# Performance work log

Measured on AMD Instinct MI355X. Metric: run time of the kernel, lower is better.

## Reference

```python
import jax, jax.numpy as jnp
import numpy as np

N, E = 50000, 400000
IN_CH, HID, HEADS, EDGE_DIM = 128, 64, 4, 3
NEG_SLOPE = 0.2


def gatv2_conv(x, src, dst, edge_attr, Wl, Wr, We, att, bias):
    # x: [N, F_in]; Wl/Wr: [H*C, F_in]; We: [H*C, edge_dim]; att: [H, C]; bias: [C]
    H, C = att.shape
    n = x.shape[0]
    xl = (x @ Wl.T).reshape(n, H, C)   # source-side transform (lin_l)
    xr = (x @ Wr.T).reshape(n, H, C)   # target-side transform (lin_r)
    e = (edge_attr @ We.T).reshape(-1, H, C)
    z = jax.nn.leaky_relu(xl[src] + xr[dst] + e, NEG_SLOPE)  # [E,H,C]
    alpha = jnp.einsum('ehc,hc->eh', z, att)                 # [E,H]
    # segment softmax over incoming edges per destination node
    amax = jax.ops.segment_max(alpha, dst, num_segments=n)
    alpha = jnp.exp(alpha - amax[dst])
    denom = jax.ops.segment_sum(alpha, dst, num_segments=n)
    alpha = alpha / (denom[dst] + 1e-16)
    msg = xl[src] * alpha[:, :, None]                        # [E,H,C]
    out = jax.ops.segment_sum(msg, dst, num_segments=n)      # [N,H,C]
    return out.mean(axis=1) + bias                           # concat=False -> head mean


def setup_inputs() -> dict:
    key = jax.random.key(0)
    ks = jax.random.split(key, 16)
    s = 0.1
    return {
        'x': jax.random.normal(ks[0], (N, IN_CH), jnp.float32),
        'edge_index': jax.random.randint(ks[1], (2, E), 0, N, jnp.int32),
        'edge_attr': jax.random.normal(ks[2], (E, EDGE_DIM), jnp.float32),
        'Wl1': jax.random.normal(ks[3], (HEADS * HID, IN_CH), jnp.float32) * s,
        'Wr1': jax.random.normal(ks[4], (HEADS * HID, IN_CH), jnp.float32) * s,
        'We1': jax.random.normal(ks[5], (HEADS * HID, EDGE_DIM), jnp.float32) * s,
        'att1': jax.random.normal(ks[6], (HEADS, HID), jnp.float32) * s,
        'b1': jnp.zeros((HID,), jnp.float32),
        'Wl2': jax.random.normal(ks[7], (HEADS * HID, HID), jnp.float32) * s,
        'Wr2': jax.random.normal(ks[8], (HEADS * HID, HID), jnp.float32) * s,
        'We2': jax.random.normal(ks[9], (HEADS * HID, EDGE_DIM), jnp.float32) * s,
        'att2': jax.random.normal(ks[10], (HEADS, HID), jnp.float32) * s,
        'b2': jnp.zeros((HID,), jnp.float32),
        'prelu_w': jnp.full((HID,), 0.25, jnp.float32),
    }


def reference(x, edge_index, edge_attr, Wl1, Wr1, We1, att1, b1, Wl2, Wr2, We2, att2, b2, prelu_w):
    src, dst = edge_index[0], edge_index[1]
    h = gatv2_conv(x, src, dst, edge_attr, Wl1, Wr1, We1, att1, b1)
    h = gatv2_conv(h, src, dst, edge_attr, Wl2, Wr2, We2, att2, b2)
    return jnp.where(h >= 0, h, prelu_w * h)  # PReLU, per-channel weight
```

## Files before the change

### kernel.cpp

```cpp
#include <hip/hip_runtime.h>
#include <hip/hip_bf16.h>

#define HC 256

typedef __attribute__((ext_vector_type(8))) short bf16x8;
typedef __attribute__((ext_vector_type(4))) float f32x4;
typedef __attribute__((ext_vector_type(2))) float f32x2;

__device__ __forceinline__ void gl_lds16(const void* g, void* l) {
  __builtin_amdgcn_global_load_lds(
      (const __attribute__((address_space(1))) unsigned int*)g,
      (__attribute__((address_space(3))) unsigned int*)l, 16, 0, 0);
}

__device__ __forceinline__ void split_w_one(const float* Wl, const float* Wr,
                                            ushort* WT, int F, int idx) {
  int col = idx / F, f = idx - col * F;
  float v = (col < 256) ? Wl[col * F + f] : Wr[(col - 256) * F + f];
  __hip_bfloat16 h = __float2bfloat16(v);
  __hip_bfloat16 l = __float2bfloat16(v - __bfloat162float(h));
  ushort* row = WT + (size_t)col * 3 * F;
  row[f] = *(ushort*)&h;
  row[F + f] = *(ushort*)&l;
  row[2 * F + f] = *(ushort*)&h;
}

__global__ void k_weights_deg(const float* __restrict__ Wl1, const float* __restrict__ Wr1,
                              ushort* __restrict__ WT1, const float* __restrict__ Wl2,
                              const float* __restrict__ Wr2, ushort* __restrict__ WT2,
                              int* __restrict__ deg, int n) {
  int idx = blockIdx.x * blockDim.x + threadIdx.x;
  const int t1 = 512 * 128, t2 = 512 * 64;
  if (idx < t1) {
    split_w_one(Wl1, Wr1, WT1, 128, idx);
  } else if (idx < t1 + t2) {
    split_w_one(Wl2, Wr2, WT2, 64, idx - t1);
  } else if (idx < t1 + t2 + n) {
    deg[idx - t1 - t2] = 0;
  }
}

template <int F>
__global__ __launch_bounds__(256) void gemm_mfma(const ushort* __restrict__ A2,
                                                 const ushort* __restrict__ WT,
                                                 ushort* __restrict__ xlb,
                                                 ushort* __restrict__ xrb, int n_nodes) {
  constexpr int KC = 3 * F;
  __shared__ __align__(16) ushort As[128 * 64];
  __shared__ __align__(16) ushort Bs[128 * 64];
  const int tid = threadIdx.x;
  const int wv = tid >> 6, lane = tid & 63;
  const int m16 = lane & 15, quad = lane >> 4;
  const int col0 = blockIdx.x * 128;
  const int row0 = blockIdx.y * 128;
  const int wm = (wv >> 1) * 64, wn = (wv & 1) * 64;
  const bool is_xl = (col0 < 256);
  const int nstep = is_xl ? (3 * F) / 64 : F / 64;

  f32x4 acc[4][4];
#pragma unroll
  for (int i = 0; i < 4; ++i)
#pragma unroll
    for (int j = 0; j < 4; ++j) acc[i][j] = (f32x4){0.f, 0.f, 0.f, 0.f};

  for (int s = 0; s < nstep; ++s) {
    const int khat = s * 64;
    const int asrc = (khat < F) ? khat : khat - F;
    __syncthreads();
#pragma unroll
    for (int t = 0; t < 4; ++t) {
      const int sl16 = tid + 256 * t;
      const int row = sl16 >> 3, sl = sl16 & 7;
      const int gch = sl ^ (row & 7);
      const int grow = row0 + row;
      if (grow < n_nodes)
        gl_lds16(A2 + (size_t)grow * (2 * F) + asrc + gch * 8, As + sl16 * 8);
      gl_lds16(WT + (size_t)(col0 + row) * KC + khat + gch * 8, Bs + sl16 * 8);
    }
    __syncthreads();
#pragma unroll
    for (int kh = 0; kh < 2; ++kh) {
      bf16x8 af[4], bf[4];
#pragma unroll
      for (int i = 0; i < 4; ++i) {
        const int row = wm + i * 16 + m16;
        const int slot = (kh * 4 + quad) ^ (row & 7);
        af[i] = *(bf16x8*)&As[row * 64 + slot * 8];
      }
#pragma unroll
      for (int j = 0; j < 4; ++j) {
        const int col = wn + j * 16 + m16;
        const int slot = (kh * 4 + quad) ^ (col & 7);
        bf[j] = *(bf16x8*)&Bs[col * 64 + slot * 8];
      }
#pragma unroll
      for (int i = 0; i < 4; ++i)
#pragma unroll
        for (int j = 0; j < 4; ++j)
          acc[i][j] =
              __builtin_amdgcn_mfma_f32_16x16x32_bf16(af[i], bf[j], acc[i][j], 0, 0, 0);
    }
  }
#pragma unroll
  for (int i = 0; i < 4; ++i) {
#pragma unroll
    for (int r = 0; r < 4; ++r) {
      const int grow = row0 + wm + i * 16 + quad * 4 + r;
      if (grow < n_nodes) {
#pragma unroll
        for (int j = 0; j < 4; ++j) {
          const float v = acc[i][j][r];
          const int col = col0 + wn + j * 16 + m16;
          __hip_bfloat16 h = __float2bfloat16(v);
          if (is_xl)
            xlb[(size_t)grow * 256 + col] = *(ushort*)&h;
          else
            xrb[(size_t)grow * 256 + (col - 256)] = *(ushort*)&h;
        }
      }
    }
  }
}

__global__ void k_hist(const int* __restrict__ ei, int* __restrict__ deg, int E_) {
  int e = blockIdx.x * blockDim.x + threadIdx.x;
  if (e < E_) atomicAdd(&deg[ei[E_ + e]], 1);
}

__global__ void k_scan_local(const int* __restrict__ deg, int* __restrict__ rowstart,
                             int* __restrict__ partial, int n) {
  __shared__ int a[256], b[256];
  const int t = threadIdx.x;
  const int i = blockIdx.x * 256 + t;
  const int v = (i < n) ? deg[i] : 0;
  a[t] = v;
  __syncthreads();
  int* cur = a;
  int* nxt = b;
  for (int off = 1; off < 256; off <<= 1) {
    int x = cur[t];
    if (t >= off) x += cur[t - off];
    nxt[t] = x;
    __syncthreads();
    int* tmp = cur; cur = nxt; nxt = tmp;
  }
  const int incl = cur[t];
  if (i < n) rowstart[i] = incl - v;
  if (t == 255) partial[blockIdx.x] = incl;
}

__global__ void k_scan_partial(int* __restrict__ partial, int nblk,
                               int* __restrict__ ssrc, float4* __restrict__ sea, int E_) {
  __shared__ int a[256], b[256];
  const int t = threadIdx.x;
  if (t < 8) {
    ssrc[E_ + t] = 0;
    sea[E_ + t] = make_float4(0.f, 0.f, 0.f, 0.f);
  }
  const int v = (t < nblk) ? partial[t] : 0;
  a[t] = v;
  __syncthreads();
  int* cur = a;
  int* nxt = b;
  for (int off = 1; off < 256; off <<= 1) {
    int x = cur[t];
    if (t >= off) x += cur[t - off];
    nxt[t] = x;
    __syncthreads();
    int* tmp = cur; cur = nxt; nxt = tmp;
  }
  if (t < nblk) partial[t] = cur[t] - v;
}

__global__ void k_add_off(int* __restrict__ rowstart, int* __restrict__ cursor,
                          const int* __restrict__ partial, int n, int E_) {
  int i = blockIdx.x * blockDim.x + threadIdx.x;
  if (i < n) {
    int v = rowstart[i] + partial[i >> 8];
    rowstart[i] = v;
    cursor[i] = v;
  }
  if (i == 0) rowstart[n] = E_;
}

__global__ void k_prep(const float* __restrict__ x, ushort* __restrict__ A2,
                       const int* __restrict__ ei, const float* __restrict__ ea,
                       int* __restrict__ cursor, int* __restrict__ ssrc,
                       float4* __restrict__ sea, int n, int E_) {
  const int nx4 = n * 128 / 4;
  int idx = blockIdx.x * blockDim.x + threadIdx.x;
  if (idx < nx4) {
    int row = idx >> 5, q = idx & 31;
    float4 v = ((const float4*)x)[idx];
    float vv[4] = {v.x, v.y, v.z, v.w};
    ushort hb[4], lb[4];
#pragma unroll
    for (int j = 0; j < 4; ++j) {
      __hip_bfloat16 h = __float2bfloat16(vv[j]);
      hb[j] = *(ushort*)&h;
      __hip_bfloat16 l = __float2bfloat16(vv[j] - __bfloat162float(h));
      lb[j] = *(ushort*)&l;
    }
    ushort* rp = A2 + (size_t)row * 256;
    *(ushort4*)(rp + q * 4) = make_ushort4(hb[0], hb[1], hb[2], hb[3]);
    *(ushort4*)(rp + 128 + q * 4) = make_ushort4(lb[0], lb[1], lb[2], lb[3]);
  } else {
    int e = idx - nx4;
    if (e < E_) {
      int dst = ei[E_ + e];
      int pos = atomicAdd(&cursor[dst], 1);
      ssrc[pos] = ei[e];
      sea[pos] = make_float4(ea[e * 3], ea[e * 3 + 1], ea[e * 3 + 2], 0.f);
    }
  }
}

__device__ __forceinline__ f32x2 vmax2(f32x2 a, f32x2 b) {
  return (f32x2){fmaxf(a.x, b.x), fmaxf(a.y, b.y)};
}
__device__ __forceinline__ f32x2 vmin2(f32x2 a, f32x2 b) {
  return (f32x2){fminf(a.x, b.x), fminf(a.y, b.y)};
}

__device__ __forceinline__ void edge_step(
    const ushort4& lu, const float4& eav, const f32x2* we0, const f32x2* we1,
    const f32x2* we2, const f32x2* at, const f32x2* xrl, f32x2& num01,
    f32x2& num23, float& den) {
  f32x2 lav0, lav1;
  lav0.x = __uint_as_float((unsigned)lu.x << 16);
  lav0.y = __uint_as_float((unsigned)lu.y << 16);
  lav1.x = __uint_as_float((unsigned)lu.z << 16);
  lav1.y = __uint_as_float((unsigned)lu.w << 16);
  const f32x2 zero = {0.f, 0.f};
  const f32x2 slope = {0.2f, 0.2f};
  f32x2 pv = zero;
#pragma unroll
  for (int j = 0; j < 2; ++j) {
    f32x2 la = (j == 0) ? lav0 : lav1;
    f32x2 ev = we0[j] * eav.x + we1[j] * eav.y + we2[j] * eav.z;
    f32x2 s = la + xrl[j] + ev;
    f32x2 z = vmax2(s, zero) + slope * vmin2(s, zero);
    pv = pv + z * at[j];
  }
  float p = pv.x + pv.y;
  p += __shfl_xor(p, 1);
  p += __shfl_xor(p, 2);
  p += __shfl_xor(p, 4);
  p += __shfl_xor(p, 8);
  const float w = __expf(p);
  den += w;
  num01 = num01 + (f32x2){w, w} * lav0;
  num23 = num23 + (f32x2){w, w} * lav1;
}

template <int MODE>
__global__ __launch_bounds__(256) void fused_attn(
    const ushort* __restrict__ xlb, const ushort* __restrict__ xrb,
    const int* __restrict__ rowstart, const int* __restrict__ ssrc,
    const float4* __restrict__ sea, const float* __restrict__ We,
    const float* __restrict__ att, const float* __restrict__ bias,
    const float* __restrict__ pw, float* __restrict__ out,
    ushort* __restrict__ outs, int n) {
  const int lane = threadIdx.x & 63;
  const int d =
      __builtin_amdgcn_readfirstlane((blockIdx.x * blockDim.x + threadIdx.x) >> 6);
  if (d >= n) return;
  f32x2 we0[2], we1[2], we2[2], at[2];
#pragma unroll
  for (int j = 0; j < 4; ++j) {
    int r = 4 * lane + j;
    ((float*)we0)[j] = We[r * 3 + 0];
    ((float*)we1)[j] = We[r * 3 + 1];
    ((float*)we2)[j] = We[r * 3 + 2];
    ((float*)at)[j] = att[r];
  }
  const ushort4* xlb4 = (const ushort4*)xlb;
  const ushort4 xu = ((const ushort4*)xrb)[(unsigned)(d * 64) + lane];
  f32x2 xrl[2];
  xrl[0].x = __uint_as_float((unsigned)xu.x << 16);
  xrl[0].y = __uint_as_float((unsigned)xu.y << 16);
  xrl[1].x = __uint_as_float((unsigned)xu.z << 16);
  xrl[1].y = __uint_as_float((unsigned)xu.w << 16);

  int pos = rowstart[d];
  const int end = rowstart[d + 1];
  f32x2 num01 = {0.f, 0.f}, num23 = {0.f, 0.f};
  float den = 0.f;

  if (pos < end) {
    int s0 = ssrc[pos], s1 = ssrc[pos + 1];
    ushort4 g0 = xlb4[(unsigned)(s0 * 64) + lane];
    ushort4 g1 = xlb4[(unsigned)(s1 * 64) + lane];
    float4 e0 = sea[pos], e1 = sea[pos + 1];
    int sn0 = ssrc[pos + 2], sn1 = ssrc[pos + 3];

    while (pos + 2 <= end) {
      ushort4 h0 = xlb4[(unsigned)(sn0 * 64) + lane];
      ushort4 h1 = xlb4[(unsigned)(sn1 * 64) + lane];
      float4 f0 = sea[pos + 2], f1 = sea[pos + 3];
      sn0 = ssrc[pos + 4];
      sn1 = ssrc[pos + 5];
      edge_step(g0, e0, we0, we1, we2, at, xrl, num01, num23, den);
      edge_step(g1, e1, we0, we1, we2, at, xrl, num01, num23, den);
      g0 = h0; g1 = h1; e0 = f0; e1 = f1;
      pos += 2;
    }
    if (pos < end)
      edge_step(g0, e0, we0, we1, we2, at, xrl, num01, num23, den);
  }

  const float inv = 1.f / (den + 1e-16f);
  float4 r;
  r.x = num01.x * inv;
  r.y = num01.y * inv;
  r.z = num23.x * inv;
  r.w = num23.y * inv;
  r.x += __shfl_xor(r.x, 16);
  r.y += __shfl_xor(r.y, 16);
  r.z += __shfl_xor(r.z, 16);
  r.w += __shfl_xor(r.w, 16);
  r.x += __shfl_xor(r.x, 32);
  r.y += __shfl_xor(r.y, 32);
  r.z += __shfl_xor(r.z, 32);
  r.w += __shfl_xor(r.w, 32);
  if (lane < 16) {
    const int c = 4 * lane;
    float o[4];
    o[0] = 0.25f * r.x + bias[c + 0];
    o[1] = 0.25f * r.y + bias[c + 1];
    o[2] = 0.25f * r.z + bias[c + 2];
    o[3] = 0.25f * r.w + bias[c + 3];
    if (MODE == 1) {
#pragma unroll
      for (int j = 0; j < 4; ++j) o[j] = (o[j] >= 0.f) ? o[j] : pw[c + j] * o[j];
      ((float4*)out)[(size_t)d * 16 + lane] = make_float4(o[0], o[1], o[2], o[3]);
    } else {
      ushort hb[4], lb[4];
#pragma unroll
      for (int j = 0; j < 4; ++j) {
        __hip_bfloat16 h = __float2bfloat16(o[j]);
        hb[j] = *(ushort*)&h;
        __hip_bfloat16 l = __float2bfloat16(o[j] - __bfloat162float(h));
        lb[j] = *(ushort*)&l;
      }
      *(ushort4*)(outs + (size_t)d * 128 + c) = make_ushort4(hb[0], hb[1], hb[2], hb[3]);
      *(ushort4*)(outs + (size_t)d * 128 + 64 + c) =
          make_ushort4(lb[0], lb[1], lb[2], lb[3]);
    }
  }
}

extern "C" void kernel_launch(void* const* d_in, const int* in_sizes, int n_in,
                              void* d_out, int out_size, void* d_ws, size_t ws_size,
                              hipStream_t stream) {
  const float* x    = (const float*)d_in[0];
  const int*   ei   = (const int*)d_in[1];
  const float* ea   = (const float*)d_in[2];
  const float* Wl1  = (const float*)d_in[3];
  const float* Wr1  = (const float*)d_in[4];
  const float* We1  = (const float*)d_in[5];
  const float* att1 = (const float*)d_in[6];
  const float* b1   = (const float*)d_in[7];
  const float* Wl2  = (const float*)d_in[8];
  const float* Wr2  = (const float*)d_in[9];
  const float* We2  = (const float*)d_in[10];
  const float* att2 = (const float*)d_in[11];
  const float* b2   = (const float*)d_in[12];
  const float* pw   = (const float*)d_in[13];
  const int N_ = in_sizes[0] / 128;
  const int E_ = in_sizes[1] / 2;
  float* out = (float*)d_out;

  char* w = (char*)d_ws;
  auto alloc = [&](size_t bytes) {
    char* p = w;
    w += (bytes + 255) & ~size_t(255);
    return p;
  };
  ushort* xlb      = (ushort*)alloc((size_t)N_ * 256 * 2);
  ushort* xrb      = (ushort*)alloc((size_t)N_ * 256 * 2);
  ushort* A2x      = (ushort*)alloc((size_t)N_ * 256 * 2);
  ushort* h2       = (ushort*)alloc((size_t)N_ * 128 * 2);
  int*    ssrc     = (int*)alloc((size_t)(E_ + 8) * 4);
  float4* sea      = (float4*)alloc((size_t)(E_ + 8) * 16);
  int*    deg      = (int*)alloc((size_t)N_ * 4);
  int*    rowstart = (int*)alloc((size_t)(N_ + 1) * 4);
  int*    cursor   = (int*)alloc((size_t)N_ * 4);
  int*    partial  = (int*)alloc(256 * 4);
  ushort* WT1      = (ushort*)alloc((size_t)512 * 384 * 2);
  ushort* WT2      = (ushort*)alloc((size_t)512 * 192 * 2);

  const int wtot = 512 * 128 + 512 * 64 + N_;
  k_weights_deg<<<(wtot + 255) / 256, 256, 0, stream>>>(Wl1, Wr1, WT1, Wl2, Wr2, WT2,
                                                        deg, N_);

  const int nblk = (N_ + 255) / 256;
  k_hist<<<(E_ + 255) / 256, 256, 0, stream>>>(ei, deg, E_);
  k_scan_local<<<nblk, 256, 0, stream>>>(deg, rowstart, partial, N_);
  k_scan_partial<<<1, 256, 0, stream>>>(partial, nblk, ssrc, sea, E_);
  k_add_off<<<nblk, 256, 0, stream>>>(rowstart, cursor, partial, N_, E_);
  const int ptot = N_ * 128 / 4 + E_;
  k_prep<<<(ptot + 255) / 256, 256, 0, stream>>>(x, A2x, ei, ea, cursor, ssrc, sea,
                                                 N_, E_);

  const dim3 GG(4, (N_ + 127) / 128);
  const int FB = (N_ + 3) / 4;

  gemm_mfma<128><<<GG, 256, 0, stream>>>(A2x, WT1, xlb, xrb, N_);
  fused_attn<0><<<FB, 256, 0, stream>>>(xlb, xrb, rowstart, ssrc, sea, We1, att1,
                                        b1, pw, nullptr, h2, N_);
  gemm_mfma<64><<<GG, 256, 0, stream>>>(h2, WT2, xlb, xrb, N_);
  fused_attn<1><<<FB, 256, 0, stream>>>(xlb, xrb, rowstart, ssrc, sea, We2, att2,
                                        b2, pw, out, nullptr, N_);
}
```

Before: 301.8 us.

## Drop split-bf16 GEMM compensation and process multiple nodes per wavefront in attention

Removes the hi/lo bf16 splitting of activations and weights, so both GEMMs run a plain single-bf16 product with a third of the K steps (layer 1) and half the A-operand traffic, and intermediate h2 is stored as single bf16. The attention kernel now launches a fixed grid of 8192 wavefronts, each looping over a chunk of destination nodes, and hoists the bias and PReLU weight loads out of the loop. The cost removed is extra MFMA work, conversion work and memory traffic, in exchange for lower numerical accuracy, which may exceed tolerance. The fixed grid also gives less latency hiding per node.

```diff
diff --git a/kernel.cpp b/kernel.cpp
--- a/kernel.cpp
+++ b/kernel.cpp
@@ -13,16 +13,12 @@
       (__attribute__((address_space(3))) unsigned int*)l, 16, 0, 0);
 }
 
-__device__ __forceinline__ void split_w_one(const float* Wl, const float* Wr,
-                                            ushort* WT, int F, int idx) {
+__device__ __forceinline__ void cast_w_one(const float* Wl, const float* Wr,
+                                           ushort* WT, int F, int idx) {
   int col = idx / F, f = idx - col * F;
   float v = (col < 256) ? Wl[col * F + f] : Wr[(col - 256) * F + f];
   __hip_bfloat16 h = __float2bfloat16(v);
-  __hip_bfloat16 l = __float2bfloat16(v - __bfloat162float(h));
-  ushort* row = WT + (size_t)col * 3 * F;
-  row[f] = *(ushort*)&h;
-  row[F + f] = *(ushort*)&l;
-  row[2 * F + f] = *(ushort*)&h;
+  WT[(size_t)col * F + f] = *(ushort*)&h;
 }
 
 __global__ void k_weights_deg(const float* __restrict__ Wl1, const float* __restrict__ Wr1,
@@ -32,20 +28,20 @@
   int idx = blockIdx.x * blockDim.x + threadIdx.x;
   const int t1 = 512 * 128, t2 = 512 * 64;
   if (idx < t1) {
-    split_w_one(Wl1, Wr1, WT1, 128, idx);
+    cast_w_one(Wl1, Wr1, WT1, 128, idx);
   } else if (idx < t1 + t2) {
-    split_w_one(Wl2, Wr2, WT2, 64, idx - t1);
+    cast_w_one(Wl2, Wr2, WT2, 64, idx - t1);
   } else if (idx < t1 + t2 + n) {
     deg[idx - t1 - t2] = 0;
   }
 }
 
 template <int F>
-__global__ __launch_bounds__(256) void gemm_mfma(const ushort* __restrict__ A2,
+__global__ __launch_bounds__(256) void gemm_mfma(const ushort* __restrict__ A,
                                                  const ushort* __restrict__ WT,
                                                  ushort* __restrict__ xlb,
                                                  ushort* __restrict__ xrb, int n_nodes) {
-  constexpr int KC = 3 * F;
+  constexpr int NSTEP = F / 64;
   __shared__ __align__(16) ushort As[128 * 64];
   __shared__ __align__(16) ushort Bs[128 * 64];
   const int tid = threadIdx.x;
@@ -54,8 +50,6 @@
   const int col0 = blockIdx.x * 128;
   const int row0 = blockIdx.y * 128;
   const int wm = (wv >> 1) * 64, wn = (wv & 1) * 64;
-  const bool is_xl = (col0 < 256);
-  const int nstep = is_xl ? (3 * F) / 64 : F / 64;
 
   f32x4 acc[4][4];
 #pragma unroll
@@ -63,9 +57,9 @@
 #pragma unroll
     for (int j = 0; j < 4; ++j) acc[i][j] = (f32x4){0.f, 0.f, 0.f, 0.f};
 
-  for (int s = 0; s < nstep; ++s) {
+#pragma unroll
+  for (int s = 0; s < NSTEP; ++s) {
     const int khat = s * 64;
-    const int asrc = (khat < F) ? khat : khat - F;
     __syncthreads();
 #pragma unroll
     for (int t = 0; t < 4; ++t) {
@@ -74,8 +68,8 @@
       const int gch = sl ^ (row & 7);
       const int grow = row0 + row;
       if (grow < n_nodes)
-        gl_lds16(A2 + (size_t)grow * (2 * F) + asrc + gch * 8, As + sl16 * 8);
-      gl_lds16(WT + (size_t)(col0 + row) * KC + khat + gch * 8, Bs + sl16 * 8);
+        gl_lds16(A + (size_t)grow * F + khat + gch * 8, As + sl16 * 8);
+      gl_lds16(WT + (size_t)(col0 + row) * F + khat + gch * 8, Bs + sl16 * 8);
     }
     __syncthreads();
 #pragma unroll
@@ -101,6 +95,7 @@
               __builtin_amdgcn_mfma_f32_16x16x32_bf16(af[i], bf[j], acc[i][j], 0, 0, 0);
     }
   }
+  const bool is_xl = (col0 < 256);
 #pragma unroll
   for (int i = 0; i < 4; ++i) {
 #pragma unroll
@@ -183,29 +178,25 @@
   if (i == 0) rowstart[n] = E_;
 }
 
-__global__ void k_prep(const float* __restrict__ x, ushort* __restrict__ A2,
+__global__ void k_prep(const float* __restrict__ x, ushort* __restrict__ A,
                        const int* __restrict__ ei, const float* __restrict__ ea,
                        int* __restrict__ cursor, int* __restrict__ ssrc,
                        float4* __restrict__ sea, int n, int E_) {
-  const int nx4 = n * 128 / 4;
+  const int nx8 = n * 16;
   int idx = blockIdx.x * blockDim.x + threadIdx.x;
-  if (idx < nx4) {
-    int row = idx >> 5, q = idx & 31;
-    float4 v = ((const float4*)x)[idx];
-    float vv[4] = {v.x, v.y, v.z, v.w};
-    ushort hb[4], lb[4];
-#pragma unroll
-    for (int j = 0; j < 4; ++j) {
+  if (idx < nx8) {
+    const float4* xp = (const float4*)x + (size_t)idx * 2;
+    float4 v0 = xp[0], v1 = xp[1];
+    float vv[8] = {v0.x, v0.y, v0.z, v0.w, v1.x, v1.y, v1.z, v1.w};
+    __align__(16) ushort hb[8];
+#pragma unroll
+    for (int j = 0; j < 8; ++j) {
       __hip_bfloat16 h = __float2bfloat16(vv[j]);
       hb[j] = *(ushort*)&h;
-      __hip_bfloat16 l = __float2bfloat16(vv[j] - __bfloat162float(h));
-      lb[j] = *(ushort*)&l;
-    }
-    ushort* rp = A2 + (size_t)row * 256;
-    *(ushort4*)(rp + q * 4) = make_ushort4(hb[0], hb[1], hb[2], hb[3]);
-    *(ushort4*)(rp + 128 + q * 4) = make_ushort4(lb[0], lb[1], lb[2], lb[3]);
+    }
+    *(int4*)(A + (size_t)idx * 8) = *(int4*)hb;
   } else {
-    int e = idx - nx4;
+    int e = idx - nx8;
     if (e < E_) {
       int dst = ei[E_ + e];
       int pos = atomicAdd(&cursor[dst], 1);
@@ -260,11 +251,14 @@
     const float4* __restrict__ sea, const float* __restrict__ We,
     const float* __restrict__ att, const float* __restrict__ bias,
     const float* __restrict__ pw, float* __restrict__ out,
-    ushort* __restrict__ outs, int n) {
+    ushort* __restrict__ outs, int n, int chunk) {
   const int lane = threadIdx.x & 63;
-  const int d =
+  const int wid =
       __builtin_amdgcn_readfirstlane((blockIdx.x * blockDim.x + threadIdx.x) >> 6);
-  if (d >= n) return;
+  const int d0 = wid * chunk;
+  if (d0 >= n) return;
+  const int d1 = min(d0 + chunk, n);
+
   f32x2 we0[2], we1[2], we2[2], at[2];
 #pragma unroll
   for (int j = 0; j < 4; ++j) {
@@ -274,78 +268,81 @@
     ((float*)we2)[j] = We[r * 3 + 2];
     ((float*)at)[j] = att[r];
   }
+  const float4 bias4 = ((const float4*)bias)[lane & 15];
+  float4 pw4 = {0.f, 0.f, 0.f, 0.f};
+  if (MODE == 1) pw4 = ((const float4*)pw)[lane & 15];
   const ushort4* xlb4 = (const ushort4*)xlb;
-  const ushort4 xu = ((const ushort4*)xrb)[(unsigned)(d * 64) + lane];
-  f32x2 xrl[2];
-  xrl[0].x = __uint_as_float((unsigned)xu.x << 16);
-  xrl[0].y = __uint_as_float((unsigned)xu.y << 16);
-  xrl[1].x = __uint_as_float((unsigned)xu.z << 16);
-  xrl[1].y = __uint_as_float((unsigned)xu.w << 16);
-
-  int pos = rowstart[d];
-  const int end = rowstart[d + 1];
-  f32x2 num01 = {0.f, 0.f}, num23 = {0.f, 0.f};
-  float den = 0.f;
-
-  if (pos < end) {
-    int s0 = ssrc[pos], s1 = ssrc[pos + 1];
-    ushort4 g0 = xlb4[(unsigned)(s0 * 64) + lane];
-    ushort4 g1 = xlb4[(unsigned)(s1 * 64) + lane];
-    float4 e0 = sea[pos], e1 = sea[pos + 1];
-    int sn0 = ssrc[pos + 2], sn1 = ssrc[pos + 3];
-
-    while (pos + 2 <= end) {
-      ushort4 h0 = xlb4[(unsigned)(sn0 * 64) + lane];
-      ushort4 h1 = xlb4[(unsigned)(sn1 * 64) + lane];
-      float4 f0 = sea[pos + 2], f1 = sea[pos + 3];
-      sn0 = ssrc[pos + 4];
-      sn1 = ssrc[pos + 5];
-      edge_step(g0, e0, we0, we1, we2, at, xrl, num01, num23, den);
-      edge_step(g1, e1, we0, we1, we2, at, xrl, num01, num23, den);
-      g0 = h0; g1 = h1; e0 = f0; e1 = f1;
-      pos += 2;
-    }
-    if (pos < end)
-      edge_step(g0, e0, we0, we1, we2, at, xrl, num01, num23, den);
-  }
-
-  const float inv = 1.f / (den + 1e-16f);
-  float4 r;
-  r.x = num01.x * inv;
-  r.y = num01.y * inv;
-  r.z = num23.x * inv;
-  r.w = num23.y * inv;
-  r.x += __shfl_xor(r.x, 16);
-  r.y += __shfl_xor(r.y, 16);
-  r.z += __shfl_xor(r.z, 16);
-  r.w += __shfl_xor(r.w, 16);
-  r.x += __shfl_xor(r.x, 32);
-  r.y += __shfl_xor(r.y, 32);
-  r.z += __shfl_xor(r.z, 32);
-  r.w += __shfl_xor(r.w, 32);
-  if (lane < 16) {
-    const int c = 4 * lane;
-    float o[4];
-    o[0] = 0.25f * r.x + bias[c + 0];
-    o[1] = 0.25f * r.y + bias[c + 1];
-    o[2] = 0.25f * r.z + bias[c + 2];
-    o[3] = 0.25f * r.w + bias[c + 3];
-    if (MODE == 1) {
-#pragma unroll
-      for (int j = 0; j < 4; ++j) o[j] = (o[j] >= 0.f) ? o[j] : pw[c + j] * o[j];
-      ((float4*)out)[(size_t)d * 16 + lane] = make_float4(o[0], o[1], o[2], o[3]);
-    } else {
-      ushort hb[4], lb[4];
-#pragma unroll
-      for (int j = 0; j < 4; ++j) {
-        __hip_bfloat16 h = __float2bfloat16(o[j]);
-        hb[j] = *(ushort*)&h;
-        __hip_bfloat16 l = __float2bfloat16(o[j] - __bfloat162float(h));
-        lb[j] = *(ushort*)&l;
+
+  for (int d = d0; d < d1; ++d) {
+    const ushort4 xu = ((const ushort4*)xrb)[(unsigned)(d * 64) + lane];
+    f32x2 xrl[2];
+    xrl[0].x = __uint_as_float((unsigned)xu.x << 16);
+    xrl[0].y = __uint_as_float((unsigned)xu.y << 16);
+    xrl[1].x = __uint_as_float((unsigned)xu.z << 16);
+    xrl[1].y = __uint_as_float((unsigned)xu.w << 16);
+
+    int pos = rowstart[d];
+    const int end = rowstart[d + 1];
+    f32x2 num01 = {0.f, 0.f}, num23 = {0.f, 0.f};
+    float den = 0.f;
+
+    if (pos < end) {
+      int s0 = ssrc[pos], s1 = ssrc[pos + 1];
+      ushort4 g0 = xlb4[(unsigned)(s0 * 64) + lane];
+      ushort4 g1 = xlb4[(unsigned)(s1 * 64) + lane];
+      float4 e0 = sea[pos], e1 = sea[pos + 1];
+      int sn0 = ssrc[pos + 2], sn1 = ssrc[pos + 3];
+
+      while (pos + 2 <= end) {
+        ushort4 h0 = xlb4[(unsigned)(sn0 * 64) + lane];
+        ushort4 h1 = xlb4[(unsigned)(sn1 * 64) + lane];
+        float4 f0 = sea[pos + 2], f1 = sea[pos + 3];
+        sn0 = ssrc[pos + 4];
+        sn1 = ssrc[pos + 5];
+        edge_step(g0, e0, we0, we1, we2, at, xrl, num01, num23, den);
+        edge_step(g1, e1, we0, we1, we2, at, xrl, num01, num23, den);
+        g0 = h0; g1 = h1; e0 = f0; e1 = f1;
+        pos += 2;
       }
-      *(ushort4*)(outs + (size_t)d * 128 + c) = make_ushort4(hb[0], hb[1], hb[2], hb[3]);
-      *(ushort4*)(outs + (size_t)d * 128 + 64 + c) =
-          make_ushort4(lb[0], lb[1], lb[2], lb[3]);
+      if (pos < end)
+        edge_step(g0, e0, we0, we1, we2, at, xrl, num01, num23, den);
+    }
+
+    const float inv = 1.f / (den + 1e-16f);
+    float4 r;
+    r.x = num01.x * inv;
+    r.y = num01.y * inv;
+    r.z = num23.x * inv;
+    r.w = num23.y * inv;
+    r.x += __shfl_xor(r.x, 16);
+    r.y += __shfl_xor(r.y, 16);
+    r.z += __shfl_xor(r.z, 16);
+    r.w += __shfl_xor(r.w, 16);
+    r.x += __shfl_xor(r.x, 32);
+    r.y += __shfl_xor(r.y, 32);
+    r.z += __shfl_xor(r.z, 32);
+    r.w += __shfl_xor(r.w, 32);
+    if (lane < 16) {
+      float o[4];
+      o[0] = 0.25f * r.x + bias4.x;
+      o[1] = 0.25f * r.y + bias4.y;
+      o[2] = 0.25f * r.z + bias4.z;
+      o[3] = 0.25f * r.w + bias4.w;
+      if (MODE == 1) {
+        const float pwv[4] = {pw4.x, pw4.y, pw4.z, pw4.w};
+#pragma unroll
+        for (int j = 0; j < 4; ++j) o[j] = (o[j] >= 0.f) ? o[j] : pwv[j] * o[j];
+        ((float4*)out)[(size_t)d * 16 + lane] = make_float4(o[0], o[1], o[2], o[3]);
+      } else {
+        ushort hb[4];
+#pragma unroll
+        for (int j = 0; j < 4; ++j) {
+          __hip_bfloat16 h = __float2bfloat16(o[j]);
+          hb[j] = *(ushort*)&h;
+        }
+        *(ushort4*)(outs + (size_t)d * 64 + 4 * lane) =
+            make_ushort4(hb[0], hb[1], hb[2], hb[3]);
+      }
     }
   }
 }
@@ -379,16 +376,16 @@
   };
   ushort* xlb      = (ushort*)alloc((size_t)N_ * 256 * 2);
   ushort* xrb      = (ushort*)alloc((size_t)N_ * 256 * 2);
-  ushort* A2x      = (ushort*)alloc((size_t)N_ * 256 * 2);
-  ushort* h2       = (ushort*)alloc((size_t)N_ * 128 * 2);
+  ushort* Ax       = (ushort*)alloc((size_t)N_ * 128 * 2);
+  ushort* h2       = (ushort*)alloc((size_t)N_ * 64 * 2);
   int*    ssrc     = (int*)alloc((size_t)(E_ + 8) * 4);
   float4* sea      = (float4*)alloc((size_t)(E_ + 8) * 16);
   int*    deg      = (int*)alloc((size_t)N_ * 4);
   int*    rowstart = (int*)alloc((size_t)(N_ + 1) * 4);
   int*    cursor   = (int*)alloc((size_t)N_ * 4);
   int*    partial  = (int*)alloc(256 * 4);
-  ushort* WT1      = (ushort*)alloc((size_t)512 * 384 * 2);
-  ushort* WT2      = (ushort*)alloc((size_t)512 * 192 * 2);
+  ushort* WT1      = (ushort*)alloc((size_t)512 * 128 * 2);
+  ushort* WT2      = (ushort*)alloc((size_t)512 * 64 * 2);
 
   const int wtot = 512 * 128 + 512 * 64 + N_;
   k_weights_deg<<<(wtot + 255) / 256, 256, 0, stream>>>(Wl1, Wr1, WT1, Wl2, Wr2, WT2,
@@ -399,17 +396,19 @@
   k_scan_local<<<nblk, 256, 0, stream>>>(deg, rowstart, partial, N_);
   k_scan_partial<<<1, 256, 0, stream>>>(partial, nblk, ssrc, sea, E_);
   k_add_off<<<nblk, 256, 0, stream>>>(rowstart, cursor, partial, N_, E_);
-  const int ptot = N_ * 128 / 4 + E_;
-  k_prep<<<(ptot + 255) / 256, 256, 0, stream>>>(x, A2x, ei, ea, cursor, ssrc, sea,
+  const int ptot = N_ * 16 + E_;
+  k_prep<<<(ptot + 255) / 256, 256, 0, stream>>>(x, Ax, ei, ea, cursor, ssrc, sea,
                                                  N_, E_);
 
   const dim3 GG(4, (N_ + 127) / 128);
-  const int FB = (N_ + 3) / 4;
-
-  gemm_mfma<128><<<GG, 256, 0, stream>>>(A2x, WT1, xlb, xrb, N_);
+  const int FW = 8192;
+  const int FB = FW / 4;
+  const int chunk = (N_ + FW - 1) / FW;
+
+  gemm_mfma<128><<<GG, 256, 0, stream>>>(Ax, WT1, xlb, xrb, N_);
   fused_attn<0><<<FB, 256, 0, stream>>>(xlb, xrb, rowstart, ssrc, sea, We1, att1,
-                                        b1, pw, nullptr, h2, N_);
+                                        b1, pw, nullptr, h2, N_, chunk);
   gemm_mfma<64><<<GG, 256, 0, stream>>>(h2, WT2, xlb, xrb, N_);
   fused_attn<1><<<FB, 256, 0, stream>>>(xlb, xrb, rowstart, ssrc, sea, We2, att2,
-                                        b2, pw, out, nullptr, N_);
-}
+                                        b2, pw, out, nullptr, N_, chunk);
+}
```

After: 280.3 us. -7.1%, faster.
